# Kernel tuning notes

Hardware: AMD Instinct MI355X
Metric: run time of the kernel (lower is better)

The kernel has to match this reference:

```python
import jax, jax.numpy as jnp
import numpy as np

MAXDISP = 192


def setup_inputs() -> dict:
    key = jax.random.key(0)
    k1, k2, k3 = jax.random.split(key, 3)
    B, C_color, D, H, W = 1, 3, MAXDISP, 192, 384
    # v: [B, 1 + C_color, D, H, W + D - 1]; channel 0 = matching cost ('block'), 1: = color
    v = jax.random.normal(k1, (B, 1 + C_color, D, H, W + D - 1), dtype=jnp.float32)
    x = jax.random.normal(k2, (B, C_color, H, W), dtype=jnp.float32)  # only supplies H, W
    y = jax.random.normal(k3, (B, C_color, H, W), dtype=jnp.float32)  # unused by forward
    return {"v": v, "x": x, "y": y}


def reference(v, x, y):
    D = MAXDISP
    B, _, H, W = x.shape
    block = v[:, 0:1]          # [B, 1, D, H, Wfull]
    color = v[:, 1:]           # [B, C, D, H, Wfull]

    # disparity values D-1 ... 0 along the disparity axis
    disp_vals = jnp.arange(D - 1, -1, -1, dtype=v.dtype).reshape(1, 1, D, 1, 1)

    # view 1: plain crop to width W
    block_1 = block[..., :W]
    color_1v = color[..., :W]
    w = jax.nn.softmax(block_1, axis=2)                 # softmax over disparity
    disp_1 = jnp.sum(w * disp_vals, axis=2)[:, 0]       # [B, H, W]
    color_1 = jnp.sum(w * color_1v, axis=2)             # [B, C, H, W]

    # view 2: per-disparity shifted crop. For disparity index d the shift is (D-1-d):
    #   out[..., d, :, w] = in[..., d, :, (D-1-d) + w]
    shift = (D - 1 - jnp.arange(D))[:, None] + jnp.arange(W)[None, :]   # [D, W]
    idx = shift.reshape(1, 1, D, 1, W)
    block_2 = jnp.take_along_axis(block, idx, axis=4)   # [B, 1, D, H, W]
    color_2v = jnp.take_along_axis(color, idx, axis=4)  # [B, C, D, H, W] (idx broadcasts)
    w2 = jax.nn.softmax(block_2, axis=2)
    disp_2 = jnp.sum(w2 * disp_vals, axis=2)[:, 0]      # [B, H, W]
    color_2 = jnp.sum(w2 * color_2v, axis=2)            # [B, C, H, W]

    return (color_1, color_2, disp_1, disp_2)
```

## Files before the change

kernel.cpp:

```cpp
#include <hip/hip_runtime.h>
#include <math.h>

#define DD 192
#define HH 192
#define WW 384
#define WV 575
#define NCHUNK 8
#define DPC 24
#define TPB 384

__global__ __launch_bounds__(TPB, 8) void vr_partial(const float* __restrict__ v,
                                                     float* __restrict__ ws) {
    const int t = threadIdx.x;
    const int h = blockIdx.x >> 3;
    const int chunk = blockIdx.x & 7;
    const int d0 = chunk * DPC;

    const size_t dstride = (size_t)HH * WV;
    const size_t cstride = (size_t)DD * dstride;

    __shared__ float rows[4][WV + 1];

    float m1 = -INFINITY, l1 = 0.f, a1 = 0.f, c10 = 0.f, c11 = 0.f, c12 = 0.f;
    float m2 = -INFINITY, l2 = 0.f, a2 = 0.f, c20 = 0.f, c21 = 0.f, c22 = 0.f;

    const float* rowbase = v + (size_t)h * WV + (size_t)d0 * dstride;
    for (int i = 0; i < DPC; ++i) {
        const int d = d0 + i;
        const int sh = (DD - 1) - d;
        const float* r = rowbase + (size_t)i * dstride;
        #pragma unroll
        for (int c = 0; c < 4; ++c) {
            const float* rc = r + (size_t)c * cstride;
            rows[c][t] = rc[t];
            if (t < WV - TPB) rows[c][t + TPB] = rc[t + TPB];
        }
        __syncthreads();

        const float b1  = rows[0][t];
        const float b2  = rows[0][t + sh];
        const float x10 = rows[1][t];
        const float x20 = rows[1][t + sh];
        const float x11 = rows[2][t];
        const float x21 = rows[2][t + sh];
        const float x12 = rows[3][t];
        const float x22 = rows[3][t + sh];
        const float dv = (float)sh;

        float nm = fmaxf(m1, b1);
        float s  = __expf(m1 - nm);
        float pr = __expf(b1 - nm);
        l1  = l1  * s + pr;
        a1  = a1  * s + pr * dv;
        c10 = c10 * s + pr * x10;
        c11 = c11 * s + pr * x11;
        c12 = c12 * s + pr * x12;
        m1 = nm;

        nm = fmaxf(m2, b2);
        s  = __expf(m2 - nm);
        pr = __expf(b2 - nm);
        l2  = l2  * s + pr;
        a2  = a2  * s + pr * dv;
        c20 = c20 * s + pr * x20;
        c21 = c21 * s + pr * x21;
        c22 = c22 * s + pr * x22;
        m2 = nm;

        __syncthreads();
    }

    float* wp = ws + (((size_t)h * NCHUNK + chunk) * 12) * WW + t;
    wp[0 * WW] = m1;  wp[1 * WW] = l1;  wp[2 * WW]  = a1;
    wp[3 * WW] = c10; wp[4 * WW] = c11; wp[5 * WW]  = c12;
    wp[6 * WW] = m2;  wp[7 * WW] = l2;  wp[8 * WW]  = a2;
    wp[9 * WW] = c20; wp[10 * WW] = c21; wp[11 * WW] = c22;
}

__global__ __launch_bounds__(256, 4) void vr_merge(const float* __restrict__ ws,
                                                   float* __restrict__ out) {
    const int pix = blockIdx.x * 256 + threadIdx.x;
    const int h = pix / WW;
    const int w = pix - h * WW;
    const int HW = HH * WW;

    #pragma unroll
    for (int pass = 0; pass < 2; ++pass) {
        float M = -INFINITY, L = 0.f, A = 0.f, C0 = 0.f, C1 = 0.f, C2 = 0.f;
        #pragma unroll
        for (int ch = 0; ch < NCHUNK; ++ch) {
            const float* q = ws + (((size_t)h * NCHUNK + ch) * 12 + pass * 6) * WW + w;
            const float mm = q[0];
            const float nm = fmaxf(M, mm);
            const float s0 = __expf(M - nm);
            const float s1 = __expf(mm - nm);
            L  = L  * s0 + q[1 * WW] * s1;
            A  = A  * s0 + q[2 * WW] * s1;
            C0 = C0 * s0 + q[3 * WW] * s1;
            C1 = C1 * s0 + q[4 * WW] * s1;
            C2 = C2 * s0 + q[5 * WW] * s1;
            M = nm;
        }
        const float inv = 1.0f / L;
        const int o = h * WW + w;
        out[(pass * 3 + 0) * HW + o] = C0 * inv;
        out[(pass * 3 + 1) * HW + o] = C1 * inv;
        out[(pass * 3 + 2) * HW + o] = C2 * inv;
        out[(6 + pass) * HW + o]     = A * inv;
    }
}

extern "C" void kernel_launch(void* const* d_in, const int* in_sizes, int n_in,
                              void* d_out, int out_size, void* d_ws, size_t ws_size,
                              hipStream_t stream) {
    const float* v = (const float*)d_in[0];
    float* out = (float*)d_out;
    float* ws = (float*)d_ws;
    vr_partial<<<HH * NCHUNK, TPB, 0, stream>>>(v, ws);
    vr_merge<<<(HH * WW) / 256, 256, 0, stream>>>(ws, out);
}
```

Baseline: 521.7 us.

## Register-prefetch disparity rows and double-buffer shared memory in partial kernel

Restructures the partial-softmax loop to load disparity rows into registers several steps ahead and stage them through a two-slot shared buffer, processing two disparities per barrier phase. Only the tail columns actually needed for the shifted view are loaded, which trims global traffic. The aim is to hide global load latency behind the exp/accumulate math and cut barriers per disparity, at the cost of more registers (launch bounds lowered to 4 waves) and more shared memory, which may reduce occupancy.

```diff
diff --git a/kernel.cpp b/kernel.cpp
--- a/kernel.cpp
+++ b/kernel.cpp
@@ -8,8 +8,9 @@
 #define NCHUNK 8
 #define DPC 24
 #define TPB 384
+#define ROUNDS 12
 
-__global__ __launch_bounds__(TPB, 8) void vr_partial(const float* __restrict__ v,
+__global__ __launch_bounds__(TPB, 4) void vr_partial(const float* __restrict__ v,
                                                      float* __restrict__ ws) {
     const int t = threadIdx.x;
     const int h = blockIdx.x >> 3;
@@ -18,62 +19,94 @@
 
     const size_t dstride = (size_t)HH * WV;
     const size_t cstride = (size_t)DD * dstride;
+    const float* base = v + (size_t)h * WV + (size_t)d0 * dstride + t;
 
-    __shared__ float rows[4][WV + 1];
+    __shared__ float rows[2][4][WV];
 
     float m1 = -INFINITY, l1 = 0.f, a1 = 0.f, c10 = 0.f, c11 = 0.f, c12 = 0.f;
     float m2 = -INFINITY, l2 = 0.f, a2 = 0.f, c20 = 0.f, c21 = 0.f, c22 = 0.f;
 
-    const float* rowbase = v + (size_t)h * WV + (size_t)d0 * dstride;
-    for (int i = 0; i < DPC; ++i) {
-        const int d = d0 + i;
-        const int sh = (DD - 1) - d;
-        const float* r = rowbase + (size_t)i * dstride;
-        #pragma unroll
-        for (int c = 0; c < 4; ++c) {
-            const float* rc = r + (size_t)c * cstride;
-            rows[c][t] = rc[t];
-            if (t < WV - TPB) rows[c][t + TPB] = rc[t + TPB];
+    float A0[4], A0t[4], A1[4], A1t[4];
+    float B0[4], B0t[4], B1[4], B1t[4];
+
+#define LOADP(M, Mt, pp) do {                                            \
+        const float* r_ = base + (size_t)(pp) * dstride;                 \
+        const int tl_ = (DD - 1) - (d0 + (pp));                          \
+        _Pragma("unroll")                                                \
+        for (int c_ = 0; c_ < 4; ++c_) {                                 \
+            M[c_] = r_[c_ * cstride];                                    \
+            if (t < tl_) Mt[c_] = r_[c_ * cstride + TPB];                \
+        } } while (0)
+
+#define STOREP(M, Mt, i, pp) do {                                        \
+        const int tl_ = (DD - 1) - (d0 + (pp));                          \
+        _Pragma("unroll")                                                \
+        for (int c_ = 0; c_ < 4; ++c_) {                                 \
+            rows[i][c_][t] = M[c_];                                      \
+            if (t < tl_) rows[i][c_][t + TPB] = Mt[c_];                  \
+        } } while (0)
+
+#define COMPUTEP(i, pp) do {                                             \
+        const int sh_ = (DD - 1) - (d0 + (pp));                          \
+        const float dv_ = (float)sh_;                                    \
+        const float b1_  = rows[i][0][t];                                \
+        const float x10_ = rows[i][1][t];                                \
+        const float x11_ = rows[i][2][t];                                \
+        const float x12_ = rows[i][3][t];                                \
+        const float b2_  = rows[i][0][t + sh_];                          \
+        const float x20_ = rows[i][1][t + sh_];                          \
+        const float x21_ = rows[i][2][t + sh_];                          \
+        const float x22_ = rows[i][3][t + sh_];                          \
+        float nm_ = fmaxf(m1, b1_);                                      \
+        float s_  = __expf(m1 - nm_);                                    \
+        float pr_ = __expf(b1_ - nm_);                                   \
+        l1  = l1  * s_ + pr_;                                            \
+        a1  = a1  * s_ + pr_ * dv_;                                      \
+        c10 = c10 * s_ + pr_ * x10_;                                     \
+        c11 = c11 * s_ + pr_ * x11_;                                     \
+        c12 = c12 * s_ + pr_ * x12_;                                     \
+        m1 = nm_;                                                        \
+        nm_ = fmaxf(m2, b2_);                                            \
+        s_  = __expf(m2 - nm_);                                          \
+        pr_ = __expf(b2_ - nm_);                                         \
+        l2  = l2  * s_ + pr_;                                            \
+        a2  = a2  * s_ + pr_ * dv_;                                      \
+        c20 = c20 * s_ + pr_ * x20_;                                     \
+        c21 = c21 * s_ + pr_ * x21_;                                     \
+        c22 = c22 * s_ + pr_ * x22_;                                     \
+        m2 = nm_;                                                        \
+    } while (0)
+
+    LOADP(A0, A0t, 0);
+    LOADP(A1, A1t, 1);
+
+    for (int r = 0; r < ROUNDS; r += 2) {
+        const int pA = r * 2;
+        const int pB = pA + 2;
+        LOADP(B0, B0t, pB);
+        LOADP(B1, B1t, pB + 1);
+        __syncthreads();
+        STOREP(A0, A0t, 0, pA);
+        STOREP(A1, A1t, 1, pA + 1);
+        __syncthreads();
+        if (r + 2 < ROUNDS) {
+            LOADP(A0, A0t, pA + 4);
+            LOADP(A1, A1t, pA + 5);
         }
+        COMPUTEP(0, pA);
+        COMPUTEP(1, pA + 1);
         __syncthreads();
-
-        const float b1  = rows[0][t];
-        const float b2  = rows[0][t + sh];
-        const float x10 = rows[1][t];
-        const float x20 = rows[1][t + sh];
-        const float x11 = rows[2][t];
-        const float x21 = rows[2][t + sh];
-        const float x12 = rows[3][t];
-        const float x22 = rows[3][t + sh];
-        const float dv = (float)sh;
-
-        float nm = fmaxf(m1, b1);
-        float s  = __expf(m1 - nm);
-        float pr = __expf(b1 - nm);
-        l1  = l1  * s + pr;
-        a1  = a1  * s + pr * dv;
-        c10 = c10 * s + pr * x10;
-        c11 = c11 * s + pr * x11;
-        c12 = c12 * s + pr * x12;
-        m1 = nm;
-
-        nm = fmaxf(m2, b2);
-        s  = __expf(m2 - nm);
-        pr = __expf(b2 - nm);
-        l2  = l2  * s + pr;
-        a2  = a2  * s + pr * dv;
-        c20 = c20 * s + pr * x20;
-        c21 = c21 * s + pr * x21;
-        c22 = c22 * s + pr * x22;
-        m2 = nm;
-
+        STOREP(B0, B0t, 0, pB);
+        STOREP(B1, B1t, 1, pB + 1);
         __syncthreads();
+        COMPUTEP(0, pB);
+        COMPUTEP(1, pB + 1);
     }
 
     float* wp = ws + (((size_t)h * NCHUNK + chunk) * 12) * WW + t;
-    wp[0 * WW] = m1;  wp[1 * WW] = l1;  wp[2 * WW]  = a1;
-    wp[3 * WW] = c10; wp[4 * WW] = c11; wp[5 * WW]  = c12;
-    wp[6 * WW] = m2;  wp[7 * WW] = l2;  wp[8 * WW]  = a2;
+    wp[0 * WW] = m1;  wp[1 * WW] = l1;   wp[2 * WW]  = a1;
+    wp[3 * WW] = c10; wp[4 * WW] = c11;  wp[5 * WW]  = c12;
+    wp[6 * WW] = m2;  wp[7 * WW] = l2;   wp[8 * WW]  = a2;
     wp[9 * WW] = c20; wp[10 * WW] = c21; wp[11 * WW] = c22;
 }
 
```

Result: no change. 525.3 us (+0.7%).

## Double-buffer LDS rows with register prefetch and batched disparity loads

Applied to the files above, without the earlier changes.

Restructures the partial kernel to load three disparities per batch into registers, prefetch the next batch while computing the current one, and double-buffer shared memory so there is one barrier per batch instead of two per disparity. It also loads only the tail columns that the shifted view actually reads (t < shift). The goal is to hide global load latency and cut synchronisation overhead. The cost is more shared memory (about 55KB) and more registers, so launch bounds drop to 4 blocks per SM, which lowers occupancy.

```diff
diff --git a/kernel.cpp b/kernel.cpp
--- a/kernel.cpp
+++ b/kernel.cpp
@@ -8,8 +8,10 @@
 #define NCHUNK 8
 #define DPC 24
 #define TPB 384
+#define BATCH 3
+#define NB (DPC / BATCH)
 
-__global__ __launch_bounds__(TPB, 8) void vr_partial(const float* __restrict__ v,
+__global__ __launch_bounds__(TPB, 4) void vr_partial(const float* __restrict__ v,
                                                      float* __restrict__ ws) {
     const int t = threadIdx.x;
     const int h = blockIdx.x >> 3;
@@ -18,62 +20,90 @@
 
     const size_t dstride = (size_t)HH * WV;
     const size_t cstride = (size_t)DD * dstride;
+    const float* base = v + (size_t)h * WV + (size_t)d0 * dstride + t;
 
-    __shared__ float rows[4][WV + 1];
+    __shared__ float rows[2][BATCH][4][WV];
 
     float m1 = -INFINITY, l1 = 0.f, a1 = 0.f, c10 = 0.f, c11 = 0.f, c12 = 0.f;
     float m2 = -INFINITY, l2 = 0.f, a2 = 0.f, c20 = 0.f, c21 = 0.f, c22 = 0.f;
 
-    const float* rowbase = v + (size_t)h * WV + (size_t)d0 * dstride;
-    for (int i = 0; i < DPC; ++i) {
-        const int d = d0 + i;
-        const int sh = (DD - 1) - d;
-        const float* r = rowbase + (size_t)i * dstride;
-        #pragma unroll
-        for (int c = 0; c < 4; ++c) {
-            const float* rc = r + (size_t)c * cstride;
-            rows[c][t] = rc[t];
-            if (t < WV - TPB) rows[c][t + TPB] = rc[t + TPB];
-        }
-        __syncthreads();
+    float R[2][BATCH][4];
+    float Rt[2][BATCH][4];
 
-        const float b1  = rows[0][t];
-        const float b2  = rows[0][t + sh];
-        const float x10 = rows[1][t];
-        const float x20 = rows[1][t + sh];
-        const float x11 = rows[2][t];
-        const float x21 = rows[2][t + sh];
-        const float x12 = rows[3][t];
-        const float x22 = rows[3][t + sh];
-        const float dv = (float)sh;
+#define LOADB(s, pb) do {                                                 \
+        _Pragma("unroll")                                                 \
+        for (int pl_ = 0; pl_ < BATCH; ++pl_) {                           \
+            const float* r_ = base + (size_t)((pb) + pl_) * dstride;      \
+            const int tl_ = (DD - 1) - (d0 + (pb) + pl_);                 \
+            _Pragma("unroll")                                             \
+            for (int c_ = 0; c_ < 4; ++c_) {                              \
+                R[s][pl_][c_] = r_[c_ * cstride];                         \
+                if (t < tl_) Rt[s][pl_][c_] = r_[c_ * cstride + TPB];     \
+            }                                                             \
+        } } while (0)
 
-        float nm = fmaxf(m1, b1);
-        float s  = __expf(m1 - nm);
-        float pr = __expf(b1 - nm);
-        l1  = l1  * s + pr;
-        a1  = a1  * s + pr * dv;
-        c10 = c10 * s + pr * x10;
-        c11 = c11 * s + pr * x11;
-        c12 = c12 * s + pr * x12;
-        m1 = nm;
+#define STOREB(s, buf, pb) do {                                           \
+        _Pragma("unroll")                                                 \
+        for (int pl_ = 0; pl_ < BATCH; ++pl_) {                           \
+            const int tl_ = (DD - 1) - (d0 + (pb) + pl_);                 \
+            _Pragma("unroll")                                             \
+            for (int c_ = 0; c_ < 4; ++c_) {                              \
+                rows[buf][pl_][c_][t] = R[s][pl_][c_];                    \
+                if (t < tl_) rows[buf][pl_][c_][t + TPB] = Rt[s][pl_][c_];\
+            }                                                             \
+        } } while (0)
 
-        nm = fmaxf(m2, b2);
-        s  = __expf(m2 - nm);
-        pr = __expf(b2 - nm);
-        l2  = l2  * s + pr;
-        a2  = a2  * s + pr * dv;
-        c20 = c20 * s + pr * x20;
-        c21 = c21 * s + pr * x21;
-        c22 = c22 * s + pr * x22;
-        m2 = nm;
+#define COMPUTEB(buf, pb) do {                                            \
+        _Pragma("unroll")                                                 \
+        for (int pl_ = 0; pl_ < BATCH; ++pl_) {                           \
+            const int sh_ = (DD - 1) - (d0 + (pb) + pl_);                 \
+            const float dv_ = (float)sh_;                                 \
+            const float b1_  = rows[buf][pl_][0][t];                      \
+            const float x10_ = rows[buf][pl_][1][t];                      \
+            const float x11_ = rows[buf][pl_][2][t];                      \
+            const float x12_ = rows[buf][pl_][3][t];                      \
+            const float b2_  = rows[buf][pl_][0][t + sh_];                \
+            const float x20_ = rows[buf][pl_][1][t + sh_];                \
+            const float x21_ = rows[buf][pl_][2][t + sh_];                \
+            const float x22_ = rows[buf][pl_][3][t + sh_];                \
+            float nm_ = fmaxf(m1, b1_);                                   \
+            float s_  = __expf(m1 - nm_);                                 \
+            float pr_ = __expf(b1_ - nm_);                                \
+            l1  = l1  * s_ + pr_;                                         \
+            a1  = a1  * s_ + pr_ * dv_;                                   \
+            c10 = c10 * s_ + pr_ * x10_;                                  \
+            c11 = c11 * s_ + pr_ * x11_;                                  \
+            c12 = c12 * s_ + pr_ * x12_;                                  \
+            m1 = nm_;                                                     \
+            nm_ = fmaxf(m2, b2_);                                         \
+            s_  = __expf(m2 - nm_);                                       \
+            pr_ = __expf(b2_ - nm_);                                      \
+            l2  = l2  * s_ + pr_;                                         \
+            a2  = a2  * s_ + pr_ * dv_;                                   \
+            c20 = c20 * s_ + pr_ * x20_;                                  \
+            c21 = c21 * s_ + pr_ * x21_;                                  \
+            c22 = c22 * s_ + pr_ * x22_;                                  \
+            m2 = nm_;                                                     \
+        } } while (0)
 
+    LOADB(0, 0);
+    STOREB(0, 0, 0);
+    __syncthreads();
+
+    #pragma unroll
+    for (int b = 0; b < NB; ++b) {
+        const int cur = b & 1;
+        const int nxt = (b + 1) & 1;
+        if (b + 1 < NB) LOADB(nxt, (b + 1) * BATCH);
+        COMPUTEB(cur, b * BATCH);
+        if (b + 1 < NB) STOREB(nxt, nxt, (b + 1) * BATCH);
         __syncthreads();
     }
 
     float* wp = ws + (((size_t)h * NCHUNK + chunk) * 12) * WW + t;
-    wp[0 * WW] = m1;  wp[1 * WW] = l1;  wp[2 * WW]  = a1;
-    wp[3 * WW] = c10; wp[4 * WW] = c11; wp[5 * WW]  = c12;
-    wp[6 * WW] = m2;  wp[7 * WW] = l2;  wp[8 * WW]  = a2;
+    wp[0 * WW] = m1;  wp[1 * WW] = l1;   wp[2 * WW]  = a1;
+    wp[3 * WW] = c10; wp[4 * WW] = c11;  wp[5 * WW]  = c12;
+    wp[6 * WW] = m2;  wp[7 * WW] = l2;   wp[8 * WW]  = a2;
     wp[9 * WW] = c20; wp[10 * WW] = c21; wp[11 * WW] = c22;
 }
 
```

Measured after the change: 461.5 us. -11.5%, faster.
